# Optimization experiments

Measured on AMD Instinct MI355X. Metric: run time of the kernel, lower is better.

The kernel has to match this reference:

```python
import jax, jax.numpy as jnp
import numpy as np

N_NODES = 40000
N_EDGES = 640000
IN_CH, HID_CH, OUT_CH = 128, 128, 64
NEG_SLOPE = 0.2  # PyG GATConv default


def _add_self_loops(src, dst, n):
    loop = jnp.arange(n, dtype=src.dtype)
    return jnp.concatenate([src, loop]), jnp.concatenate([dst, loop])


def gcn_conv(x, src, dst, W, b, n):
    # PyG GCNConv: add self-loops, symmetric degree norm, then aggregate.
    h = x @ W                                   # [N, F_out]
    s, d = _add_self_loops(src, dst, n)
    deg = jax.ops.segment_sum(jnp.ones_like(d, dtype=h.dtype), d, num_segments=n)
    dinv = jnp.where(deg > 0, jax.lax.rsqrt(deg), 0.0)
    norm = dinv[s] * dinv[d]                    # [E+N]
    msg = h[s] * norm[:, None]                  # gather + scale
    out = jax.ops.segment_sum(msg, d, num_segments=n)
    return out + b


def gat_conv(x, src, dst, W, a_src, a_dst, b, n):
    # PyG GATConv, heads=1: self-loops, edge-wise LeakyReLU attention logits,
    # softmax over incoming edges per dst node, weighted scatter-add.
    h = x @ W                                   # [N, F_out]
    s, d = _add_self_loops(src, dst, n)
    logit = jax.nn.leaky_relu((h @ a_src)[s] + (h @ a_dst)[d], NEG_SLOPE)  # [E+N]
    mx = jax.ops.segment_max(logit, d, num_segments=n)
    e = jnp.exp(logit - mx[d])
    z = jax.ops.segment_sum(e, d, num_segments=n)
    alpha = e / z[d]
    out = jax.ops.segment_sum(h[s] * alpha[:, None], d, num_segments=n)
    return out + b


def setup_inputs() -> dict:
    key = jax.random.key(0)
    ks = jax.random.split(key, 16)
    x = jax.random.normal(ks[0], (N_NODES, IN_CH), dtype=jnp.float32)
    edge_index = jax.random.randint(ks[1], (2, N_EDGES), 0, N_NODES, dtype=jnp.int64 if jax.config.jax_enable_x64 else jnp.int32)
    glorot = lambda k, fi, fo: jax.random.normal(k, (fi, fo), jnp.float32) * np.sqrt(2.0 / (fi + fo))
    params = {
        'W1': glorot(ks[2], IN_CH, HID_CH),   'b1': jnp.zeros((HID_CH,), jnp.float32),
        'Wg1': glorot(ks[3], HID_CH, HID_CH), 'ag1_src': jax.random.normal(ks[4], (HID_CH,), jnp.float32) * 0.1,
        'ag1_dst': jax.random.normal(ks[5], (HID_CH,), jnp.float32) * 0.1, 'bg1': jnp.zeros((HID_CH,), jnp.float32),
        'W2': glorot(ks[6], HID_CH, OUT_CH),  'b2': jnp.zeros((OUT_CH,), jnp.float32),
        'Wg2': glorot(ks[7], OUT_CH, OUT_CH), 'ag2_src': jax.random.normal(ks[8], (OUT_CH,), jnp.float32) * 0.1,
        'ag2_dst': jax.random.normal(ks[9], (OUT_CH,), jnp.float32) * 0.1, 'bg2': jnp.zeros((OUT_CH,), jnp.float32),
    }
    return {'x': x, 'edge_index': edge_index, **params}


def reference(x, edge_index, W1, b1, Wg1, ag1_src, ag1_dst, bg1, W2, b2, Wg2, ag2_src, ag2_dst, bg2):
    n = x.shape[0]
    src, dst = edge_index[0], edge_index[1]
    h = jax.nn.relu(gcn_conv(x, src, dst, W1, b1, n))
    # dropout(p=0.5) is identity in eval mode
    encoded = gat_conv(h, src, dst, Wg1, ag1_src, ag1_dst, bg1, n)
    h = jax.nn.relu(gcn_conv(encoded, src, dst, W2, b2, n))
    decoded = gat_conv(h, src, dst, Wg2, ag2_src, ag2_dst, bg2, n)
    return encoded, decoded
```

## Files before the change

### kernel.cpp

```cpp
#include <hip/hip_runtime.h>

#define NN 40000
#define NE 640000
#define NSB ((NN + 255) / 256)
#define NNP (NN + 64)

typedef unsigned int uint32;
typedef unsigned short ushort;
typedef __attribute__((ext_vector_type(8))) short bf16x8;
typedef __attribute__((ext_vector_type(4))) float f32x4;

static __device__ __forceinline__ float lrelu(float x) { return x > 0.0f ? x : 0.2f * x; }

static __device__ __forceinline__ float wave_max(float v) {
    for (int off = 32; off; off >>= 1) v = fmaxf(v, __shfl_xor(v, off));
    return v;
}
static __device__ __forceinline__ float wave_sum(float v) {
    for (int off = 32; off; off >>= 1) v += __shfl_xor(v, off);
    return v;
}

static __device__ __forceinline__ uint32 bfr(float x) {
    uint32 u = __float_as_uint(x);
    return u + 0x7FFFu + ((u >> 16) & 1u);
}
static __device__ __forceinline__ ushort bf16of(float x) { return (ushort)(bfr(x) >> 16); }
static __device__ __forceinline__ uint32 pack2(float a, float b) {
    return (bfr(a) >> 16) | (bfr(b) & 0xFFFF0000u);
}
static __device__ __forceinline__ float lo16(uint32 v) { return __uint_as_float(v << 16); }
static __device__ __forceinline__ float hi16(uint32 v) { return __uint_as_float(v & 0xFFFF0000u); }

__global__ void k_xcast(const float* __restrict__ x, ushort* __restrict__ xb) {
    int i = blockIdx.x * blockDim.x + threadIdx.x;
    int base = i * 4;
    if (base < NN * 128) {
        float4 v = *(const float4*)&x[base];
        ushort4 o;
        o.x = bf16of(v.x);
        o.y = bf16of(v.y);
        o.z = bf16of(v.z);
        o.w = bf16of(v.w);
        *(ushort4*)&xb[base] = o;
    }
}
__global__ void k_wcast(const float* __restrict__ W1, const float* __restrict__ Wg1,
                        const float* __restrict__ W2, const float* __restrict__ Wg2,
                        ushort* __restrict__ t1, ushort* __restrict__ tg1,
                        ushort* __restrict__ t2, ushort* __restrict__ tg2) {
    const float* W;
    ushort* T;
    int K, N;
    switch (blockIdx.y) {
        case 0: W = W1; T = t1; K = 128; N = 128; break;
        case 1: W = Wg1; T = tg1; K = 128; N = 128; break;
        case 2: W = W2; T = t2; K = 128; N = 64; break;
        default: W = Wg2; T = tg2; K = 64; N = 64; break;
    }
    int idx = blockIdx.x * 256 + threadIdx.x;
    if (idx < K * N) {
        int n = idx / K, k = idx % K;
        T[idx] = bf16of(W[k * N + n]);
    }
}

template <int FIN, int FOUT, bool WF32>
__global__ __launch_bounds__(256) void k_gemm_mfma(const ushort* __restrict__ Xb,
                                                   const ushort* __restrict__ Wt,
                                                   float* __restrict__ Y,
                                                   ushort* __restrict__ Y16) {
    constexpr int NT = FOUT / 16;
    const int w = threadIdx.x >> 6, lane = threadIdx.x & 63;
    const int row0 = blockIdx.x * 128 + w * 32;
    const int lr = lane & 15;
    const int lk = (lane >> 4) * 8;

    f32x4 acc[2][NT];
#pragma unroll
    for (int mt = 0; mt < 2; ++mt)
#pragma unroll
        for (int nt = 0; nt < NT; ++nt) acc[mt][nt] = (f32x4){0.f, 0.f, 0.f, 0.f};

#pragma unroll
    for (int ks = 0; ks < FIN / 32; ++ks) {
        bf16x8 a[2], b[NT];
#pragma unroll
        for (int mt = 0; mt < 2; ++mt)
            a[mt] = *(const bf16x8*)&Xb[(size_t)(row0 + mt * 16 + lr) * FIN + ks * 32 + lk];
#pragma unroll
        for (int nt = 0; nt < NT; ++nt)
            b[nt] = *(const bf16x8*)&Wt[(size_t)(nt * 16 + lr) * FIN + ks * 32 + lk];
#pragma unroll
        for (int mt = 0; mt < 2; ++mt)
#pragma unroll
            for (int nt = 0; nt < NT; ++nt)
                acc[mt][nt] =
                    __builtin_amdgcn_mfma_f32_16x16x32_bf16(a[mt], b[nt], acc[mt][nt], 0, 0, 0);
    }

    const int rbase = (lane >> 4) * 4;
#pragma unroll
    for (int mt = 0; mt < 2; ++mt)
#pragma unroll
        for (int nt = 0; nt < NT; ++nt) {
            int col = nt * 16 + lr;
#pragma unroll
            for (int i = 0; i < 4; ++i) {
                int r = row0 + mt * 16 + rbase + i;
                if (r < NN) {
                    float v = acc[mt][nt][i];
                    if (WF32) Y[(size_t)r * FOUT + col] = v;
                    Y16[(size_t)r * FOUT + col] = bf16of(v);
                }
            }
        }
}

__global__ void k_zero_int(int* __restrict__ p, int n) {
    int i = blockIdx.x * blockDim.x + threadIdx.x;
    if (i < n) p[i] = 0;
}
__global__ void k_count(const int* __restrict__ dst, int* __restrict__ cnt) {
    int e = blockIdx.x * blockDim.x + threadIdx.x;
    if (e < NE) atomicAdd(&cnt[dst[e]], 1);
}
__global__ void k_bsum(const int* __restrict__ cnt, int* __restrict__ bsum) {
    __shared__ int wsums[4];
    int i = blockIdx.x * 256 + threadIdx.x;
    int v = (i < NN) ? cnt[i] : 0;
    for (int off = 32; off; off >>= 1) v += __shfl_down(v, off);
    if ((threadIdx.x & 63) == 0) wsums[threadIdx.x >> 6] = v;
    __syncthreads();
    if (threadIdx.x == 0) bsum[blockIdx.x] = wsums[0] + wsums[1] + wsums[2] + wsums[3];
}
__global__ void k_scanpart(const int* __restrict__ bsum, int* __restrict__ bofs,
                           int* __restrict__ rowptr) {
    __shared__ int s[256];
    int t = threadIdx.x;
    int v = (t < NSB) ? bsum[t] : 0;
    s[t] = v;
    __syncthreads();
    for (int off = 1; off < 256; off <<= 1) {
        int u = (t >= off) ? s[t - off] : 0;
        __syncthreads();
        s[t] += u;
        __syncthreads();
    }
    if (t < NSB) bofs[t] = s[t] - v;
    if (t == 0) rowptr[NN] = NE;
}
__global__ void k_scatter(const int* __restrict__ cnt, const int* __restrict__ bofs,
                          int* __restrict__ rowptr, int* __restrict__ cursor,
                          float* __restrict__ dinv) {
    __shared__ int wsums[4];
    int t = threadIdx.x;
    int lane = t & 63, w = t >> 6;
    int i = blockIdx.x * 256 + t;
    int v = (i < NN) ? cnt[i] : 0;
    int x = v;
    for (int off = 1; off < 64; off <<= 1) {
        int u = __shfl_up(x, off);
        if (lane >= off) x += u;
    }
    if (lane == 63) wsums[w] = x;
    __syncthreads();
    int wofs = 0;
    for (int k = 0; k < w; ++k) wofs += wsums[k];
    int excl = bofs[blockIdx.x] + wofs + x - v;
    if (i < NN) {
        rowptr[i] = excl;
        cursor[i] = excl;
        dinv[i] = rsqrtf(1.0f + (float)v);
    }
}
__global__ void k_fill(const int* __restrict__ src, const int* __restrict__ dst,
                       int* __restrict__ cursor, int* __restrict__ csr_src) {
    int e = blockIdx.x * blockDim.x + threadIdx.x;
    if (e < NE) {
        int p = atomicAdd(&cursor[dst[e]], 1);
        csr_src[p] = src[e];
    }
}

static __device__ __forceinline__ void gath128(const uint32* __restrict__ h16, int lane, int myi,
                                               float myw, int cnt, float* acc) {
    for (int j = 0; j < cnt; j += 8) {
        int s[8];
        float w[8];
#pragma unroll
        for (int u = 0; u < 8; ++u) {
            s[u] = __shfl(myi, j + u);
            w[u] = __shfl(myw, j + u);
        }
        uint32 v[8];
#pragma unroll
        for (int u = 0; u < 8; ++u) v[u] = h16[(size_t)s[u] * 64 + lane];
#pragma unroll
        for (int u = 0; u < 8; ++u) {
            acc[0] = fmaf(w[u], lo16(v[u]), acc[0]);
            acc[1] = fmaf(w[u], hi16(v[u]), acc[1]);
        }
    }
}
static __device__ __forceinline__ void gath64(const uint32* __restrict__ h16, int lane, int myi,
                                              float myw, int cnt, float* acc) {
    int hh = lane >> 5, cl = lane & 31;
    for (int j = 0; j < cnt; j += 16) {
        int s[8];
        float w[8];
#pragma unroll
        for (int u = 0; u < 8; ++u) {
            int e = j + 2 * u + hh;
            s[u] = __shfl(myi, e);
            w[u] = __shfl(myw, e);
        }
        uint32 v[8];
#pragma unroll
        for (int u = 0; u < 8; ++u) v[u] = h16[(size_t)s[u] * 32 + cl];
#pragma unroll
        for (int u = 0; u < 8; ++u) {
            acc[0] = fmaf(w[u], lo16(v[u]), acc[0]);
            acc[1] = fmaf(w[u], hi16(v[u]), acc[1]);
        }
    }
}

template <int F>
__global__ __launch_bounds__(256) void k_gcn_gather_w(const int* __restrict__ rowptr,
                                                      const int* __restrict__ csr_src,
                                                      const uint32* __restrict__ h16,
                                                      const float* __restrict__ dinv,
                                                      const float* __restrict__ b,
                                                      uint32* __restrict__ out16) {
    int node = blockIdx.x * 4 + (threadIdx.x >> 6);
    int lane = threadIdx.x & 63;
    int beg = rowptr[node], end = rowptr[node + 1];
    float dd = dinv[node];
    float acc[2] = {0.0f, 0.0f};

    for (int g = beg; g < end; g += 64) {
        int cnt = end - g;
        if (cnt > 64) cnt = 64;
        int myi = node;
        float myw = 0.0f;
        if (lane < cnt) {
            int s = csr_src[g + lane];
            myi = s;
            myw = dinv[s];
        }
        if (F == 128)
            gath128(h16, lane, myi, myw, cnt, acc);
        else
            gath64(h16, lane, myi, myw, cnt, acc);
    }
    if (F == 128) {
        uint32 sv = h16[(size_t)node * 64 + lane];
        acc[0] = fmaf(dd, lo16(sv), acc[0]);
        acc[1] = fmaf(dd, hi16(sv), acc[1]);
        int c = lane * 2;
        float rx = fmaxf(fmaf(acc[0], dd, b[c]), 0.0f);
        float ry = fmaxf(fmaf(acc[1], dd, b[c + 1]), 0.0f);
        out16[(size_t)node * 64 + lane] = pack2(rx, ry);
    } else {
        acc[0] += __shfl_xor(acc[0], 32);
        acc[1] += __shfl_xor(acc[1], 32);
        if (lane < 32) {
            uint32 sv = h16[(size_t)node * 32 + lane];
            acc[0] = fmaf(dd, lo16(sv), acc[0]);
            acc[1] = fmaf(dd, hi16(sv), acc[1]);
            int c = lane * 2;
            float rx = fmaxf(fmaf(acc[0], dd, b[c]), 0.0f);
            float ry = fmaxf(fmaf(acc[1], dd, b[c + 1]), 0.0f);
            out16[(size_t)node * 32 + lane] = pack2(rx, ry);
        }
    }
}

__global__ void k_gat_scalars(const float* __restrict__ hg, const float* __restrict__ a_s,
                              const float* __restrict__ a_d, float* __restrict__ asrc,
                              float* __restrict__ adst, int F) {
    int node = blockIdx.x * (blockDim.x >> 6) + (threadIdx.x >> 6);
    int lane = threadIdx.x & 63;
    if (node >= NN) return;
    float s = 0.0f, d = 0.0f;
    for (int c = lane; c < F; c += 64) {
        float v = hg[(size_t)node * F + c];
        s += v * a_s[c];
        d += v * a_d[c];
    }
    for (int off = 32; off; off >>= 1) {
        s += __shfl_down(s, off);
        d += __shfl_down(d, off);
    }
    if (lane == 0) {
        asrc[node] = s;
        adst[node] = d;
    }
}

template <int F, bool WB16>
__global__ __launch_bounds__(256) void k_gat_gather_w(const int* __restrict__ rowptr,
                                                      const int* __restrict__ csr_src,
                                                      const uint32* __restrict__ h16,
                                                      const float* __restrict__ asrc,
                                                      const float* __restrict__ adst,
                                                      const float* __restrict__ b,
                                                      float* __restrict__ out,
                                                      uint32* __restrict__ out16) {
    int node = blockIdx.x * 4 + (threadIdx.x >> 6);
    int lane = threadIdx.x & 63;
    int beg = rowptr[node], end = rowptr[node + 1];
    int deg = end - beg;
    float ad = adst[node];
    float slog = lrelu(asrc[node] + ad);
    float acc[2] = {0.0f, 0.0f};
    float wself;

    if (deg <= 64) {
        int myi = node;
        float logit = -1e30f;
        if (lane < deg) {
            myi = csr_src[beg + lane];
            logit = lrelu(asrc[myi] + ad);
        }
        float m = fmaxf(slog, wave_max(logit));
        float e = (lane < deg) ? __expf(logit - m) : 0.0f;
        float z = wave_sum(e) + __expf(slog - m);
        float zi = 1.0f / z;
        float myw = e * zi;
        wself = __expf(slog - m) * zi;
        if (F == 128)
            gath128(h16, lane, myi, myw, deg, acc);
        else
            gath64(h16, lane, myi, myw, deg, acc);
    } else {
        float lm = slog;
        for (int j = beg + lane; j < end; j += 64) lm = fmaxf(lm, lrelu(asrc[csr_src[j]] + ad));
        float m = wave_max(lm);
        float lz = 0.0f;
        for (int j = beg + lane; j < end; j += 64)
            lz += __expf(lrelu(asrc[csr_src[j]] + ad) - m);
        float z = wave_sum(lz) + __expf(slog - m);
        float zi = 1.0f / z;
        wself = __expf(slog - m) * zi;
        for (int g = beg; g < end; g += 64) {
            int cnt = end - g;
            if (cnt > 64) cnt = 64;
            int myi = node;
            float myw = 0.0f;
            if (lane < cnt) {
                int s = csr_src[g + lane];
                myi = s;
                myw = __expf(lrelu(asrc[s] + ad) - m) * zi;
            }
            if (F == 128)
                gath128(h16, lane, myi, myw, cnt, acc);
            else
                gath64(h16, lane, myi, myw, cnt, acc);
        }
    }
    if (F == 128) {
        uint32 sv = h16[(size_t)node * 64 + lane];
        acc[0] = fmaf(wself, lo16(sv), acc[0]);
        acc[1] = fmaf(wself, hi16(sv), acc[1]);
        int c = lane * 2;
        float2 r;
        r.x = acc[0] + b[c];
        r.y = acc[1] + b[c + 1];
        *(float2*)&out[(size_t)node * 128 + c] = r;
        if (WB16) out16[(size_t)node * 64 + lane] = pack2(r.x, r.y);
    } else {
        acc[0] += __shfl_xor(acc[0], 32);
        acc[1] += __shfl_xor(acc[1], 32);
        if (lane < 32) {
            uint32 sv = h16[(size_t)node * 32 + lane];
            acc[0] = fmaf(wself, lo16(sv), acc[0]);
            acc[1] = fmaf(wself, hi16(sv), acc[1]);
            int c = lane * 2;
            float2 r;
            r.x = acc[0] + b[c];
            r.y = acc[1] + b[c + 1];
            *(float2*)&out[(size_t)node * 64 + c] = r;
            if (WB16) out16[(size_t)node * 32 + lane] = pack2(r.x, r.y);
        }
    }
}

extern "C" void kernel_launch(void* const* d_in, const int* in_sizes, int n_in,
                              void* d_out, int out_size, void* d_ws, size_t ws_size,
                              hipStream_t stream) {
    const float* x = (const float*)d_in[0];
    const int* src = (const int*)d_in[1];
    const int* dst = src + NE;
    const float* W1 = (const float*)d_in[2];
    const float* b1 = (const float*)d_in[3];
    const float* Wg1 = (const float*)d_in[4];
    const float* ag1s = (const float*)d_in[5];
    const float* ag1d = (const float*)d_in[6];
    const float* bg1 = (const float*)d_in[7];
    const float* W2 = (const float*)d_in[8];
    const float* b2 = (const float*)d_in[9];
    const float* Wg2 = (const float*)d_in[10];
    const float* ag2s = (const float*)d_in[11];
    const float* ag2d = (const float*)d_in[12];
    const float* bg2 = (const float*)d_in[13];

    float* enc = (float*)d_out;
    float* dec = enc + (size_t)NN * 128;

    float* bufA = (float*)d_ws;
    ushort* ush = (ushort*)(bufA + (size_t)NN * 128);
    ushort* m0 = ush;
    ushort* m1 = m0 + (size_t)NNP * 128;
    ushort* m2 = m1 + (size_t)NNP * 128;
    ushort* wt1 = m2 + (size_t)NNP * 128;
    ushort* wtg1 = wt1 + 128 * 128;
    ushort* wt2 = wtg1 + 128 * 128;
    ushort* wtg2 = wt2 + 64 * 128;
    float* dinv = (float*)(wtg2 + 64 * 64);
    float* asrc = dinv + NN;
    float* adst = asrc + NN;
    int* cnt = (int*)(adst + NN);
    int* rowptr = cnt + NN;
    int* cursor = rowptr + NN + 1;
    int* csr_src = cursor + NN;
    int* bsum = csr_src + NE;
    int* bofs = bsum + NSB;

    const int TB = 256;
    int gN = (NN + TB - 1) / TB;
    int gE = (NE + TB - 1) / TB;
    int gScal = (NN + 3) / 4;
    int gWave = NN / 4;
    int gM = (NN + 127) / 128;

    k_xcast<<<(NN * 128 / 4 + TB - 1) / TB, TB, 0, stream>>>(x, m0);
    k_wcast<<<dim3(64, 4), TB, 0, stream>>>(W1, Wg1, W2, Wg2, wt1, wtg1, wt2, wtg2);

    k_zero_int<<<gN, TB, 0, stream>>>(cnt, NN);
    k_count<<<gE, TB, 0, stream>>>(dst, cnt);
    k_bsum<<<NSB, 256, 0, stream>>>(cnt, bsum);
    k_scanpart<<<1, 256, 0, stream>>>(bsum, bofs, rowptr);
    k_scatter<<<NSB, 256, 0, stream>>>(cnt, bofs, rowptr, cursor, dinv);
    k_fill<<<gE, TB, 0, stream>>>(src, dst, cursor, csr_src);

    k_gemm_mfma<128, 128, false><<<gM, 256, 0, stream>>>(m0, wt1, bufA, m2);
    k_gcn_gather_w<128><<<gWave, 256, 0, stream>>>(rowptr, csr_src, (uint32*)m2, dinv, b1,
                                                   (uint32*)m1);

    k_gemm_mfma<128, 128, true><<<gM, 256, 0, stream>>>(m1, wtg1, bufA, m2);
    k_gat_scalars<<<gScal, TB, 0, stream>>>(bufA, ag1s, ag1d, asrc, adst, 128);
    k_gat_gather_w<128, true><<<gWave, 256, 0, stream>>>(rowptr, csr_src, (uint32*)m2, asrc,
                                                         adst, bg1, enc, (uint32*)m0);

    k_gemm_mfma<128, 64, false><<<gM, 256, 0, stream>>>(m0, wt2, bufA, m2);
    k_gcn_gather_w<64><<<gWave, 256, 0, stream>>>(rowptr, csr_src, (uint32*)m2, dinv, b2,
                                                  (uint32*)m1);

    k_gemm_mfma<64, 64, true><<<gM, 256, 0, stream>>>(m1, wtg2, bufA, m2);
    k_gat_scalars<<<gScal, TB, 0, stream>>>(bufA, ag2s, ag2d, asrc, adst, 64);
    k_gat_gather_w<64, false><<<gWave, 256, 0, stream>>>(rowptr, csr_src, (uint32*)m2, asrc,
                                                         adst, bg2, dec, (uint32*)m0);
}
```

Baseline: 241.2 us.

## Fuse GAT attention scalars into GEMM epilogue and merge cast kernels

Computes the per-node GAT source and destination attention dot products inside the MFMA GEMM epilogue with 16-lane shuffle reductions. This removes the fp32 GEMM output buffer and the separate scalar kernel that re-read it. It also merges the x and weight cast kernels into one launch and marks csr_src loads as nontemporal. Attention logits now come from fp32 accumulators directly, which matches the old fp32 path.

```diff
diff --git a/kernel.cpp b/kernel.cpp
--- a/kernel.cpp
+++ b/kernel.cpp
@@ -32,30 +32,31 @@
 static __device__ __forceinline__ float lo16(uint32 v) { return __uint_as_float(v << 16); }
 static __device__ __forceinline__ float hi16(uint32 v) { return __uint_as_float(v & 0xFFFF0000u); }
 
-__global__ void k_xcast(const float* __restrict__ x, ushort* __restrict__ xb) {
-    int i = blockIdx.x * blockDim.x + threadIdx.x;
-    int base = i * 4;
-    if (base < NN * 128) {
-        float4 v = *(const float4*)&x[base];
-        ushort4 o;
-        o.x = bf16of(v.x);
-        o.y = bf16of(v.y);
-        o.z = bf16of(v.z);
-        o.w = bf16of(v.w);
-        *(ushort4*)&xb[base] = o;
-    }
-}
-__global__ void k_wcast(const float* __restrict__ W1, const float* __restrict__ Wg1,
-                        const float* __restrict__ W2, const float* __restrict__ Wg2,
-                        ushort* __restrict__ t1, ushort* __restrict__ tg1,
-                        ushort* __restrict__ t2, ushort* __restrict__ tg2) {
+__global__ void k_cast(const float* __restrict__ x, ushort* __restrict__ xb,
+                       const float* __restrict__ W1, const float* __restrict__ Wg1,
+                       const float* __restrict__ W2, const float* __restrict__ Wg2,
+                       ushort* __restrict__ t1, ushort* __restrict__ tg1,
+                       ushort* __restrict__ t2, ushort* __restrict__ tg2) {
+    if (blockIdx.y == 0) {
+        int base = (blockIdx.x * 256 + threadIdx.x) * 4;
+        if (base < NN * 128) {
+            float4 v = *(const float4*)&x[base];
+            ushort4 o;
+            o.x = bf16of(v.x);
+            o.y = bf16of(v.y);
+            o.z = bf16of(v.z);
+            o.w = bf16of(v.w);
+            *(ushort4*)&xb[base] = o;
+        }
+        return;
+    }
     const float* W;
     ushort* T;
     int K, N;
     switch (blockIdx.y) {
-        case 0: W = W1; T = t1; K = 128; N = 128; break;
-        case 1: W = Wg1; T = tg1; K = 128; N = 128; break;
-        case 2: W = W2; T = t2; K = 128; N = 64; break;
+        case 1: W = W1; T = t1; K = 128; N = 128; break;
+        case 2: W = Wg1; T = tg1; K = 128; N = 128; break;
+        case 3: W = W2; T = t2; K = 128; N = 64; break;
         default: W = Wg2; T = tg2; K = 64; N = 64; break;
     }
     int idx = blockIdx.x * 256 + threadIdx.x;
@@ -65,11 +66,14 @@
     }
 }
 
-template <int FIN, int FOUT, bool WF32>
+template <int FIN, int FOUT, bool GAT>
 __global__ __launch_bounds__(256) void k_gemm_mfma(const ushort* __restrict__ Xb,
                                                    const ushort* __restrict__ Wt,
-                                                   float* __restrict__ Y,
-                                                   ushort* __restrict__ Y16) {
+                                                   ushort* __restrict__ Y16,
+                                                   const float* __restrict__ a_s,
+                                                   const float* __restrict__ a_d,
+                                                   float* __restrict__ asrc,
+                                                   float* __restrict__ adst) {
     constexpr int NT = FOUT / 16;
     const int w = threadIdx.x >> 6, lane = threadIdx.x & 63;
     const int row0 = blockIdx.x * 128 + w * 32;
@@ -108,13 +112,36 @@
 #pragma unroll
             for (int i = 0; i < 4; ++i) {
                 int r = row0 + mt * 16 + rbase + i;
-                if (r < NN) {
+                if (r < NN) Y16[(size_t)r * FOUT + col] = bf16of(acc[mt][nt][i]);
+            }
+        }
+
+    if (GAT) {
+#pragma unroll
+        for (int mt = 0; mt < 2; ++mt)
+#pragma unroll
+            for (int i = 0; i < 4; ++i) {
+                float ss = 0.0f, dd = 0.0f;
+#pragma unroll
+                for (int nt = 0; nt < NT; ++nt) {
                     float v = acc[mt][nt][i];
-                    if (WF32) Y[(size_t)r * FOUT + col] = v;
-                    Y16[(size_t)r * FOUT + col] = bf16of(v);
+                    ss = fmaf(v, a_s[nt * 16 + lr], ss);
+                    dd = fmaf(v, a_d[nt * 16 + lr], dd);
+                }
+#pragma unroll
+                for (int off = 1; off < 16; off <<= 1) {
+                    ss += __shfl_xor(ss, off);
+                    dd += __shfl_xor(dd, off);
+                }
+                if (lr == 0) {
+                    int r = row0 + mt * 16 + rbase + i;
+                    if (r < NN) {
+                        asrc[r] = ss;
+                        adst[r] = dd;
+                    }
                 }
             }
-        }
+    }
 }
 
 __global__ void k_zero_int(int* __restrict__ p, int n) {
@@ -245,7 +272,7 @@
         int myi = node;
         float myw = 0.0f;
         if (lane < cnt) {
-            int s = csr_src[g + lane];
+            int s = __builtin_nontemporal_load(&csr_src[g + lane]);
             myi = s;
             myw = dinv[s];
         }
@@ -277,28 +304,6 @@
     }
 }
 
-__global__ void k_gat_scalars(const float* __restrict__ hg, const float* __restrict__ a_s,
-                              const float* __restrict__ a_d, float* __restrict__ asrc,
-                              float* __restrict__ adst, int F) {
-    int node = blockIdx.x * (blockDim.x >> 6) + (threadIdx.x >> 6);
-    int lane = threadIdx.x & 63;
-    if (node >= NN) return;
-    float s = 0.0f, d = 0.0f;
-    for (int c = lane; c < F; c += 64) {
-        float v = hg[(size_t)node * F + c];
-        s += v * a_s[c];
-        d += v * a_d[c];
-    }
-    for (int off = 32; off; off >>= 1) {
-        s += __shfl_down(s, off);
-        d += __shfl_down(d, off);
-    }
-    if (lane == 0) {
-        asrc[node] = s;
-        adst[node] = d;
-    }
-}
-
 template <int F, bool WB16>
 __global__ __launch_bounds__(256) void k_gat_gather_w(const int* __restrict__ rowptr,
                                                       const int* __restrict__ csr_src,
@@ -321,7 +326,7 @@
         int myi = node;
         float logit = -1e30f;
         if (lane < deg) {
-            myi = csr_src[beg + lane];
+            myi = __builtin_nontemporal_load(&csr_src[beg + lane]);
             logit = lrelu(asrc[myi] + ad);
         }
         float m = fmaxf(slog, wave_max(logit));
@@ -409,9 +414,7 @@
     float* enc = (float*)d_out;
     float* dec = enc + (size_t)NN * 128;
 
-    float* bufA = (float*)d_ws;
-    ushort* ush = (ushort*)(bufA + (size_t)NN * 128);
-    ushort* m0 = ush;
+    ushort* m0 = (ushort*)d_ws;
     ushort* m1 = m0 + (size_t)NNP * 128;
     ushort* m2 = m1 + (size_t)NNP * 128;
     ushort* wt1 = m2 + (size_t)NNP * 128;
@@ -431,12 +434,11 @@
     const int TB = 256;
     int gN = (NN + TB - 1) / TB;
     int gE = (NE + TB - 1) / TB;
-    int gScal = (NN + 3) / 4;
     int gWave = NN / 4;
     int gM = (NN + 127) / 128;
 
-    k_xcast<<<(NN * 128 / 4 + TB - 1) / TB, TB, 0, stream>>>(x, m0);
-    k_wcast<<<dim3(64, 4), TB, 0, stream>>>(W1, Wg1, W2, Wg2, wt1, wtg1, wt2, wtg2);
+    k_cast<<<dim3((NN * 128 / 4 + TB - 1) / TB, 5), TB, 0, stream>>>(x, m0, W1, Wg1, W2, Wg2,
+                                                                     wt1, wtg1, wt2, wtg2);
 
     k_zero_int<<<gN, TB, 0, stream>>>(cnt, NN);
     k_count<<<gE, TB, 0, stream>>>(dst, cnt);
@@ -445,21 +447,21 @@
     k_scatter<<<NSB, 256, 0, stream>>>(cnt, bofs, rowptr, cursor, dinv);
     k_fill<<<gE, TB, 0, stream>>>(src, dst, cursor, csr_src);
 
-    k_gemm_mfma<128, 128, false><<<gM, 256, 0, stream>>>(m0, wt1, bufA, m2);
+    k_gemm_mfma<128, 128, false><<<gM, 256, 0, stream>>>(m0, wt1, m2, nullptr, nullptr, nullptr,
+                                                         nullptr);
     k_gcn_gather_w<128><<<gWave, 256, 0, stream>>>(rowptr, csr_src, (uint32*)m2, dinv, b1,
                                                    (uint32*)m1);
 
-    k_gemm_mfma<128, 128, true><<<gM, 256, 0, stream>>>(m1, wtg1, bufA, m2);
-    k_gat_scalars<<<gScal, TB, 0, stream>>>(bufA, ag1s, ag1d, asrc, adst, 128);
+    k_gemm_mfma<128, 128, true><<<gM, 256, 0, stream>>>(m1, wtg1, m2, ag1s, ag1d, asrc, adst);
     k_gat_gather_w<128, true><<<gWave, 256, 0, stream>>>(rowptr, csr_src, (uint32*)m2, asrc,
                                                          adst, bg1, enc, (uint32*)m0);
 
-    k_gemm_mfma<128, 64, false><<<gM, 256, 0, stream>>>(m0, wt2, bufA, m2);
+    k_gemm_mfma<128, 64, false><<<gM, 256, 0, stream>>>(m0, wt2, m2, nullptr, nullptr, nullptr,
+                                                        nullptr);
     k_gcn_gather_w<64><<<gWave, 256, 0, stream>>>(rowptr, csr_src, (uint32*)m2, dinv, b2,
                                                   (uint32*)m1);
 
-    k_gemm_mfma<64, 64, true><<<gM, 256, 0, stream>>>(m1, wtg2, bufA, m2);
-    k_gat_scalars<<<gScal, TB, 0, stream>>>(bufA, ag2s, ag2d, asrc, adst, 64);
+    k_gemm_mfma<64, 64, true><<<gM, 256, 0, stream>>>(m1, wtg2, m2, ag2s, ag2d, asrc, adst);
     k_gat_gather_w<64, false><<<gWave, 256, 0, stream>>>(rowptr, csr_src, (uint32*)m2, asrc,
                                                          adst, bg2, dec, (uint32*)m0);
 }
```

Result: faster. 235.2 us (-2.5%).
